# Optimization experiments

Hardware: AMD Instinct MI355X
Metric: run time of the kernel (lower is better)

## Reference

```python
import jax, jax.numpy as jnp
import numpy as np

EPS = 1e-8


def setup_inputs() -> dict:
    key = jax.random.key(0)
    k1, k2, k3 = jax.random.split(key, 3)
    N, M, D = 200000, 64, 128
    X = jax.random.normal(k1, (N, D), dtype=jnp.float32)
    r = jax.random.uniform(k2, (N, M), dtype=jnp.float32)
    mus = jax.random.normal(k3, (M, D), dtype=jnp.float32)
    return {"X": X, "r": r, "mus": mus}


def _pairwise_l2_sim(X, mus):
    # sim = -||x - mu||_2, computed via the Gram trick to avoid an [N,M,D] intermediate
    x2 = jnp.sum(X * X, axis=-1, keepdims=True)          # [N,1]
    m2 = jnp.sum(mus * mus, axis=-1)[None, :]            # [1,M]
    sq = x2 + m2 - 2.0 * (X @ mus.T)                     # [N,M]
    return -jnp.sqrt(jnp.maximum(sq, 0.0))


def reference(X, r, mus):
    N = X.shape[0]
    sim = _pairwise_l2_sim(X, mus)                       # [N,M]
    sim_z = -jnp.log(jax.nn.sigmoid(sim) + EPS)          # [N,M]
    loss = jnp.sum(r * sim_z) / N
    return loss
```

## Files before the change

kernel.cpp:

```cpp
#include <hip/hip_runtime.h>
#include <math.h>

#define D_DIM 128
#define M_CLUSTERS 64
#define BLOCK 256
#define GRIDB 1024
#define W_TOTAL 4096
#define RBLOCK 1024

typedef __bf16 bf16x8 __attribute__((ext_vector_type(8)));
typedef float f32x4 __attribute__((ext_vector_type(4)));

union B8 { int4 i; bf16x8 b; };
union F4 { float4 v; float f[4]; };

__device__ __forceinline__ float zval(float sq) {
    float dd = sqrtf(fmaxf(sq, 0.0f));
    float sg = __fdividef(1.0f, 1.0f + __expf(dd));
    return -__logf(sg + 1e-8f);
}

__device__ __forceinline__ void gload16(const void* g, void* l) {
    __builtin_amdgcn_global_load_lds(
        (const __attribute__((address_space(1))) unsigned int*)g,
        (__attribute__((address_space(3))) unsigned int*)l, 16, 0, 0);
}

__global__ void iso_prep(const float4* __restrict__ mus4, int4* __restrict__ muB4,
                         float* __restrict__ m2) {
    const int f = blockIdx.x * 256 + threadIdx.x;
    float4 v0 = mus4[f * 2 + 0];
    float4 v1 = mus4[f * 2 + 1];
    B8 p;
    p.b[0] = (__bf16)v0.x; p.b[1] = (__bf16)v0.y;
    p.b[2] = (__bf16)v0.z; p.b[3] = (__bf16)v0.w;
    p.b[4] = (__bf16)v1.x; p.b[5] = (__bf16)v1.y;
    p.b[6] = (__bf16)v1.z; p.b[7] = (__bf16)v1.w;
    muB4[f] = p.i;
    if (blockIdx.x == 0 && threadIdx.x < M_CLUSTERS) {
        const float4* mv = mus4 + threadIdx.x * (D_DIM / 4);
        float s = 0.f;
#pragma unroll
        for (int d = 0; d < D_DIM / 4; ++d) {
            float4 v = mv[d];
            s = fmaf(v.x, v.x, s);
            s = fmaf(v.y, v.y, s);
            s = fmaf(v.z, v.z, s);
            s = fmaf(v.w, v.w, s);
        }
        m2[threadIdx.x] = s;
    }
}

__global__ __launch_bounds__(BLOCK, 4) void iso_main(
        const float* __restrict__ X, const float* __restrict__ r,
        const int4* __restrict__ muB4, const float* __restrict__ m2g,
        float* __restrict__ partials, int N) {
    __shared__ __align__(16) char bs[16384];

    const int tid = threadIdx.x;
    const int lane = tid & 63;
    const int la = lane & 15;
    const int lg = lane >> 4;
    const int w = tid >> 6;
    const int gid = blockIdx.x * 4 + w;
    const int ntiles = N >> 4;

#pragma unroll
    for (int i = 0; i < 4; ++i) {
        int kchunk = w * 4 + i;
        int c = kchunk * 4 + (lane >> 4);
        int slot = (lane & 15) ^ (c & 7);
        gload16(muB4 + c * 16 + slot, bs + kchunk * 1024);
    }
    F4 m2r[4];
    {
        const float4* mp = (const float4*)m2g + lg;
#pragma unroll
        for (int cb = 0; cb < 4; ++cb) m2r[cb].v = mp[cb * 4];
    }
    float4 xA[8], xB[8];
    {
        const char* xb = (const char*)X + (size_t)gid * 8192 +
                         (size_t)la * 512 + lg * 32;
        xA[0] = *(const float4*)(xb + 0);   xA[1] = *(const float4*)(xb + 16);
        xA[2] = *(const float4*)(xb + 128); xA[3] = *(const float4*)(xb + 144);
        xA[4] = *(const float4*)(xb + 256); xA[5] = *(const float4*)(xb + 272);
        xA[6] = *(const float4*)(xb + 384); xA[7] = *(const float4*)(xb + 400);
    }
    __syncthreads();

    float partial = 0.f;

    auto run_stage = [&](int k, const float4 (&cur)[8], float4 (&nxt)[8]) {
        const int tk = gid + k * W_TOTAL;
        const bool valid = tk < ntiles;
        const size_t ta = valid ? (size_t)tk : (size_t)gid;

        F4 rv[4];
        const char* rb = (const char*)r + ta * 4096 + (size_t)la * 256 + lg * 16;
        rv[0].v = *(const float4*)(rb + 0);
        rv[1].v = *(const float4*)(rb + 64);
        rv[2].v = *(const float4*)(rb + 128);
        rv[3].v = *(const float4*)(rb + 192);

        int tn = gid + (k + 1) * W_TOTAL;
        if (tn >= ntiles) tn = gid;
        const char* xb = (const char*)X + (size_t)tn * 8192 +
                         (size_t)la * 512 + lg * 32;
        nxt[0] = *(const float4*)(xb + 0);   nxt[1] = *(const float4*)(xb + 16);
        nxt[2] = *(const float4*)(xb + 128); nxt[3] = *(const float4*)(xb + 144);
        nxt[4] = *(const float4*)(xb + 256); nxt[5] = *(const float4*)(xb + 272);
        nxt[6] = *(const float4*)(xb + 384); nxt[7] = *(const float4*)(xb + 400);

        __builtin_amdgcn_sched_barrier(0);

        B8 xf[4];
        float x2 = 0.f;
#pragma unroll
        for (int kk = 0; kk < 4; ++kk) {
            float4 a = cur[2 * kk], b = cur[2 * kk + 1];
            xf[kk].b[0] = (__bf16)a.x; xf[kk].b[1] = (__bf16)a.y;
            xf[kk].b[2] = (__bf16)a.z; xf[kk].b[3] = (__bf16)a.w;
            xf[kk].b[4] = (__bf16)b.x; xf[kk].b[5] = (__bf16)b.y;
            xf[kk].b[6] = (__bf16)b.z; xf[kk].b[7] = (__bf16)b.w;
            x2 = fmaf(a.x, a.x, x2); x2 = fmaf(a.y, a.y, x2);
            x2 = fmaf(a.z, a.z, x2); x2 = fmaf(a.w, a.w, x2);
            x2 = fmaf(b.x, b.x, x2); x2 = fmaf(b.y, b.y, x2);
            x2 = fmaf(b.z, b.z, x2); x2 = fmaf(b.w, b.w, x2);
        }

        f32x4 acc[4];
#pragma unroll
        for (int cb = 0; cb < 4; ++cb)
#pragma unroll
            for (int q = 0; q < 4; ++q) acc[cb][q] = 0.f;
#pragma unroll
        for (int kk = 0; kk < 4; ++kk)
#pragma unroll
            for (int cb = 0; cb < 4; ++cb) {
                int c = cb * 16 + la;
                B8 bfr;
                bfr.i = *(const int4*)(bs + c * 256 +
                                       (((kk * 4 + lg) ^ (c & 7)) * 16));
                acc[cb] = __builtin_amdgcn_mfma_f32_16x16x32_bf16(
                    bfr.b, xf[kk].b, acc[cb], 0, 0, 0);
            }

        x2 += __shfl_xor(x2, 16, 64);
        x2 += __shfl_xor(x2, 32, 64);

        float p = 0.f;
#pragma unroll
        for (int cb = 0; cb < 4; ++cb)
#pragma unroll
            for (int q = 0; q < 4; ++q) {
                float sq = x2 + m2r[cb].f[q] - 2.0f * acc[cb][q];
                p = fmaf(rv[cb].f[q], zval(sq), p);
            }
        if (valid) partial += p;
    };

    run_stage(0, xA, xB);
    run_stage(1, xB, xA);
    run_stage(2, xA, xB);
    run_stage(3, xB, xA);

#pragma unroll
    for (int off = 32; off > 0; off >>= 1)
        partial += __shfl_down(partial, off, 64);
    if (lane == 0) partials[gid] = partial;
}

__global__ __launch_bounds__(RBLOCK) void iso_reduce(
        const float* __restrict__ partials, int n,
        float* __restrict__ out, float invN) {
    float s = 0.f;
    for (int i = threadIdx.x; i < n; i += RBLOCK) s += partials[i];
#pragma unroll
    for (int off = 32; off > 0; off >>= 1)
        s += __shfl_down(s, off, 64);
    __shared__ float wsum[RBLOCK / 64];
    const int lane = threadIdx.x & 63;
    const int wid = threadIdx.x >> 6;
    if (lane == 0) wsum[wid] = s;
    __syncthreads();
    if (threadIdx.x == 0) {
        float t = 0.f;
#pragma unroll
        for (int j = 0; j < RBLOCK / 64; ++j) t += wsum[j];
        out[0] = t * invN;
    }
}

extern "C" void kernel_launch(void* const* d_in, const int* in_sizes, int n_in,
                              void* d_out, int out_size, void* d_ws, size_t ws_size,
                              hipStream_t stream) {
    const float* X = (const float*)d_in[0];
    const float* r = (const float*)d_in[1];
    const float* mus = (const float*)d_in[2];
    const int N = in_sizes[0] / D_DIM;

    int4* muB4 = (int4*)d_ws;
    float* m2 = (float*)((char*)d_ws + 16384);
    float* partials = m2 + M_CLUSTERS;

    hipLaunchKernelGGL(iso_prep, dim3(4), dim3(256), 0, stream,
                       (const float4*)mus, muB4, m2);
    hipLaunchKernelGGL(iso_main, dim3(GRIDB), dim3(BLOCK), 0, stream,
                       X, r, muB4, m2, partials, N);
    hipLaunchKernelGGL(iso_reduce, dim3(1), dim3(RBLOCK), 0, stream,
                       partials, W_TOTAL, (float*)d_out, 1.0f / (float)N);
}
```

Before: 41.32 us.

## Fuse prep and reduce into main kernel with last-block atomic reduction

Each block now converts mus to bf16 into LDS and computes the squared norms itself, which removes the separate prep kernel. The final sum is done by the last block to finish, detected with an atomic counter, which removes the separate reduce kernel. The last stage also stops issuing the useless X prefetch. Every block repeats the 32KB mus conversion, and a memset launch is added to reset the counter.

```diff
diff --git a/kernel.cpp b/kernel.cpp
--- a/kernel.cpp
+++ b/kernel.cpp
@@ -6,7 +6,6 @@
 #define BLOCK 256
 #define GRIDB 1024
 #define W_TOTAL 4096
-#define RBLOCK 1024
 
 typedef __bf16 bf16x8 __attribute__((ext_vector_type(8)));
 typedef float f32x4 __attribute__((ext_vector_type(4)));
@@ -20,65 +19,22 @@
     return -__logf(sg + 1e-8f);
 }
 
-__device__ __forceinline__ void gload16(const void* g, void* l) {
-    __builtin_amdgcn_global_load_lds(
-        (const __attribute__((address_space(1))) unsigned int*)g,
-        (__attribute__((address_space(3))) unsigned int*)l, 16, 0, 0);
-}
-
-__global__ void iso_prep(const float4* __restrict__ mus4, int4* __restrict__ muB4,
-                         float* __restrict__ m2) {
-    const int f = blockIdx.x * 256 + threadIdx.x;
-    float4 v0 = mus4[f * 2 + 0];
-    float4 v1 = mus4[f * 2 + 1];
-    B8 p;
-    p.b[0] = (__bf16)v0.x; p.b[1] = (__bf16)v0.y;
-    p.b[2] = (__bf16)v0.z; p.b[3] = (__bf16)v0.w;
-    p.b[4] = (__bf16)v1.x; p.b[5] = (__bf16)v1.y;
-    p.b[6] = (__bf16)v1.z; p.b[7] = (__bf16)v1.w;
-    muB4[f] = p.i;
-    if (blockIdx.x == 0 && threadIdx.x < M_CLUSTERS) {
-        const float4* mv = mus4 + threadIdx.x * (D_DIM / 4);
-        float s = 0.f;
-#pragma unroll
-        for (int d = 0; d < D_DIM / 4; ++d) {
-            float4 v = mv[d];
-            s = fmaf(v.x, v.x, s);
-            s = fmaf(v.y, v.y, s);
-            s = fmaf(v.z, v.z, s);
-            s = fmaf(v.w, v.w, s);
-        }
-        m2[threadIdx.x] = s;
-    }
-}
-
 __global__ __launch_bounds__(BLOCK, 4) void iso_main(
         const float* __restrict__ X, const float* __restrict__ r,
-        const int4* __restrict__ muB4, const float* __restrict__ m2g,
-        float* __restrict__ partials, int N) {
-    __shared__ __align__(16) char bs[16384];
+        const float4* __restrict__ mus4, float* __restrict__ partials,
+        unsigned int* __restrict__ cnt, float* __restrict__ out,
+        int N, float invN) {
+    __shared__ __align__(16) char bs[16384 + 256];
+    __shared__ float wsum[4];
+    __shared__ unsigned int isLast;
 
     const int tid = threadIdx.x;
     const int lane = tid & 63;
     const int la = lane & 15;
     const int lg = lane >> 4;
-    const int w = tid >> 6;
-    const int gid = blockIdx.x * 4 + w;
+    const int gid = blockIdx.x * 4 + (tid >> 6);
     const int ntiles = N >> 4;
 
-#pragma unroll
-    for (int i = 0; i < 4; ++i) {
-        int kchunk = w * 4 + i;
-        int c = kchunk * 4 + (lane >> 4);
-        int slot = (lane & 15) ^ (c & 7);
-        gload16(muB4 + c * 16 + slot, bs + kchunk * 1024);
-    }
-    F4 m2r[4];
-    {
-        const float4* mp = (const float4*)m2g + lg;
-#pragma unroll
-        for (int cb = 0; cb < 4; ++cb) m2r[cb].v = mp[cb * 4];
-    }
     float4 xA[8], xB[8];
     {
         const char* xb = (const char*)X + (size_t)gid * 8192 +
@@ -88,11 +44,43 @@
         xA[4] = *(const float4*)(xb + 256); xA[5] = *(const float4*)(xb + 272);
         xA[6] = *(const float4*)(xb + 384); xA[7] = *(const float4*)(xb + 400);
     }
+
+    {
+        float msq = 0.f;
+#pragma unroll
+        for (int i = 0; i < 4; ++i) {
+            int f = tid * 4 + i;
+            int c = f >> 4, sl = f & 15;
+            float4 v0 = mus4[f * 2 + 0];
+            float4 v1 = mus4[f * 2 + 1];
+            B8 p;
+            p.b[0] = (__bf16)v0.x; p.b[1] = (__bf16)v0.y;
+            p.b[2] = (__bf16)v0.z; p.b[3] = (__bf16)v0.w;
+            p.b[4] = (__bf16)v1.x; p.b[5] = (__bf16)v1.y;
+            p.b[6] = (__bf16)v1.z; p.b[7] = (__bf16)v1.w;
+            *(int4*)(bs + c * 256 + ((sl ^ (c & 7)) * 16)) = p.i;
+            msq = fmaf(v0.x, v0.x, msq); msq = fmaf(v0.y, v0.y, msq);
+            msq = fmaf(v0.z, v0.z, msq); msq = fmaf(v0.w, v0.w, msq);
+            msq = fmaf(v1.x, v1.x, msq); msq = fmaf(v1.y, v1.y, msq);
+            msq = fmaf(v1.z, v1.z, msq); msq = fmaf(v1.w, v1.w, msq);
+        }
+        msq += __shfl_xor(msq, 1, 64);
+        msq += __shfl_xor(msq, 2, 64);
+        if ((tid & 3) == 0)
+            ((float*)(bs + 16384))[tid >> 2] = msq;
+    }
     __syncthreads();
 
+    F4 m2r[4];
+    {
+        const float4* m2p = (const float4*)(bs + 16384);
+#pragma unroll
+        for (int cb = 0; cb < 4; ++cb) m2r[cb].v = m2p[cb * 4 + lg];
+    }
+
     float partial = 0.f;
 
-    auto run_stage = [&](int k, const float4 (&cur)[8], float4 (&nxt)[8]) {
+    auto run_stage = [&](int k, bool pf, const float4 (&cur)[8], float4 (&nxt)[8]) {
         const int tk = gid + k * W_TOTAL;
         const bool valid = tk < ntiles;
         const size_t ta = valid ? (size_t)tk : (size_t)gid;
@@ -104,15 +92,21 @@
         rv[2].v = *(const float4*)(rb + 128);
         rv[3].v = *(const float4*)(rb + 192);
 
-        int tn = gid + (k + 1) * W_TOTAL;
-        if (tn >= ntiles) tn = gid;
-        const char* xb = (const char*)X + (size_t)tn * 8192 +
-                         (size_t)la * 512 + lg * 32;
-        nxt[0] = *(const float4*)(xb + 0);   nxt[1] = *(const float4*)(xb + 16);
-        nxt[2] = *(const float4*)(xb + 128); nxt[3] = *(const float4*)(xb + 144);
-        nxt[4] = *(const float4*)(xb + 256); nxt[5] = *(const float4*)(xb + 272);
-        nxt[6] = *(const float4*)(xb + 384); nxt[7] = *(const float4*)(xb + 400);
-
+        if (pf) {
+            int tn = gid + (k + 1) * W_TOTAL;
+            if (tn < ntiles) {
+                const char* xb = (const char*)X + (size_t)tn * 8192 +
+                                 (size_t)la * 512 + lg * 32;
+                nxt[0] = *(const float4*)(xb + 0);
+                nxt[1] = *(const float4*)(xb + 16);
+                nxt[2] = *(const float4*)(xb + 128);
+                nxt[3] = *(const float4*)(xb + 144);
+                nxt[4] = *(const float4*)(xb + 256);
+                nxt[5] = *(const float4*)(xb + 272);
+                nxt[6] = *(const float4*)(xb + 384);
+                nxt[7] = *(const float4*)(xb + 400);
+            }
+        }
         __builtin_amdgcn_sched_barrier(0);
 
         B8 xf[4];
@@ -161,35 +155,36 @@
         if (valid) partial += p;
     };
 
-    run_stage(0, xA, xB);
-    run_stage(1, xB, xA);
-    run_stage(2, xA, xB);
-    run_stage(3, xB, xA);
+    run_stage(0, true, xA, xB);
+    run_stage(1, true, xB, xA);
+    run_stage(2, true, xA, xB);
+    run_stage(3, false, xB, xA);
 
 #pragma unroll
     for (int off = 32; off > 0; off >>= 1)
         partial += __shfl_down(partial, off, 64);
     if (lane == 0) partials[gid] = partial;
-}
-
-__global__ __launch_bounds__(RBLOCK) void iso_reduce(
-        const float* __restrict__ partials, int n,
-        float* __restrict__ out, float invN) {
-    float s = 0.f;
-    for (int i = threadIdx.x; i < n; i += RBLOCK) s += partials[i];
-#pragma unroll
-    for (int off = 32; off > 0; off >>= 1)
-        s += __shfl_down(s, off, 64);
-    __shared__ float wsum[RBLOCK / 64];
-    const int lane = threadIdx.x & 63;
-    const int wid = threadIdx.x >> 6;
-    if (lane == 0) wsum[wid] = s;
+
+    __threadfence();
     __syncthreads();
-    if (threadIdx.x == 0) {
-        float t = 0.f;
-#pragma unroll
-        for (int j = 0; j < RBLOCK / 64; ++j) t += wsum[j];
-        out[0] = t * invN;
+    if (tid == 0) {
+        unsigned int old = atomicAdd(cnt, 1u);
+        isLast = (old == GRIDB - 1) ? 1u : 0u;
+    }
+    __syncthreads();
+    if (isLast) {
+        __threadfence();
+        float s = 0.f;
+        for (int i = tid; i < W_TOTAL; i += BLOCK) s += partials[i];
+#pragma unroll
+        for (int off = 32; off > 0; off >>= 1)
+            s += __shfl_down(s, off, 64);
+        if (lane == 0) wsum[tid >> 6] = s;
+        __syncthreads();
+        if (tid == 0) {
+            out[0] = (wsum[0] + wsum[1] + wsum[2] + wsum[3]) * invN;
+            *cnt = 0;
+        }
     }
 }
 
@@ -201,14 +196,11 @@
     const float* mus = (const float*)d_in[2];
     const int N = in_sizes[0] / D_DIM;
 
-    int4* muB4 = (int4*)d_ws;
-    float* m2 = (float*)((char*)d_ws + 16384);
-    float* partials = m2 + M_CLUSTERS;
-
-    hipLaunchKernelGGL(iso_prep, dim3(4), dim3(256), 0, stream,
-                       (const float4*)mus, muB4, m2);
+    float* partials = (float*)d_ws;
+    unsigned int* cnt = (unsigned int*)((char*)d_ws + W_TOTAL * sizeof(float));
+
+    hipMemsetAsync(cnt, 0, sizeof(unsigned int), stream);
     hipLaunchKernelGGL(iso_main, dim3(GRIDB), dim3(BLOCK), 0, stream,
-                       X, r, muB4, m2, partials, N);
-    hipLaunchKernelGGL(iso_reduce, dim3(1), dim3(RBLOCK), 0, stream,
-                       partials, W_TOTAL, (float*)d_out, 1.0f / (float)N);
+                       X, r, (const float4*)mus, partials, cnt, (float*)d_out,
+                       N, 1.0f / (float)N);
 }
```

Result: slower. 150.8 us, median of 6 (+264.9%).

## Double waves per block and drop register prefetch of next X tile

Applied to the files above, without the earlier changes.

Doubles the block to 8 waves and the total wave count to 8192, so each wave handles 2 tiles instead of 4. The explicit register double-buffering of the next X tile and the sched_barrier are removed, and tiles are loaded inside a simple loop with an early break. The m2 values are staged through shared memory instead of being held in registers across the kernel. The intent is to lower register pressure and raise occupancy so latency is hidden by more resident waves rather than by software prefetch, at the cost of less per-wave overlap of loads with compute.

```diff
diff --git a/kernel.cpp b/kernel.cpp
--- a/kernel.cpp
+++ b/kernel.cpp
@@ -3,9 +3,9 @@
 
 #define D_DIM 128
 #define M_CLUSTERS 64
-#define BLOCK 256
+#define BLOCK 512
 #define GRIDB 1024
-#define W_TOTAL 4096
+#define W_TOTAL 8192
 #define RBLOCK 1024
 
 typedef __bf16 bf16x8 __attribute__((ext_vector_type(8)));
@@ -52,74 +52,57 @@
     }
 }
 
-__global__ __launch_bounds__(BLOCK, 4) void iso_main(
+__global__ __launch_bounds__(BLOCK, 8) void iso_main(
         const float* __restrict__ X, const float* __restrict__ r,
         const int4* __restrict__ muB4, const float* __restrict__ m2g,
         float* __restrict__ partials, int N) {
-    __shared__ __align__(16) char bs[16384];
+    __shared__ __align__(16) char bs[16384 + 256];
 
     const int tid = threadIdx.x;
     const int lane = tid & 63;
     const int la = lane & 15;
     const int lg = lane >> 4;
     const int w = tid >> 6;
-    const int gid = blockIdx.x * 4 + w;
+    const int gid = blockIdx.x * 8 + w;
     const int ntiles = N >> 4;
 
 #pragma unroll
-    for (int i = 0; i < 4; ++i) {
-        int kchunk = w * 4 + i;
+    for (int i = 0; i < 2; ++i) {
+        int kchunk = w * 2 + i;
         int c = kchunk * 4 + (lane >> 4);
         int slot = (lane & 15) ^ (c & 7);
         gload16(muB4 + c * 16 + slot, bs + kchunk * 1024);
     }
-    F4 m2r[4];
-    {
-        const float4* mp = (const float4*)m2g + lg;
-#pragma unroll
-        for (int cb = 0; cb < 4; ++cb) m2r[cb].v = mp[cb * 4];
-    }
-    float4 xA[8], xB[8];
-    {
-        const char* xb = (const char*)X + (size_t)gid * 8192 +
-                         (size_t)la * 512 + lg * 32;
-        xA[0] = *(const float4*)(xb + 0);   xA[1] = *(const float4*)(xb + 16);
-        xA[2] = *(const float4*)(xb + 128); xA[3] = *(const float4*)(xb + 144);
-        xA[4] = *(const float4*)(xb + 256); xA[5] = *(const float4*)(xb + 272);
-        xA[6] = *(const float4*)(xb + 384); xA[7] = *(const float4*)(xb + 400);
-    }
+    if (tid < M_CLUSTERS) ((float*)(bs + 16384))[tid] = m2g[tid];
     __syncthreads();
 
     float partial = 0.f;
 
-    auto run_stage = [&](int k, const float4 (&cur)[8], float4 (&nxt)[8]) {
+    for (int k = 0; k < 2; ++k) {
         const int tk = gid + k * W_TOTAL;
-        const bool valid = tk < ntiles;
-        const size_t ta = valid ? (size_t)tk : (size_t)gid;
+        if (tk >= ntiles) break;
+
+        const char* xb = (const char*)X + (size_t)tk * 8192 +
+                         (size_t)la * 512 + lg * 32;
+        float4 xv[8];
+        xv[0] = *(const float4*)(xb + 0);   xv[1] = *(const float4*)(xb + 16);
+        xv[2] = *(const float4*)(xb + 128); xv[3] = *(const float4*)(xb + 144);
+        xv[4] = *(const float4*)(xb + 256); xv[5] = *(const float4*)(xb + 272);
+        xv[6] = *(const float4*)(xb + 384); xv[7] = *(const float4*)(xb + 400);
 
         F4 rv[4];
-        const char* rb = (const char*)r + ta * 4096 + (size_t)la * 256 + lg * 16;
+        const char* rb = (const char*)r + (size_t)tk * 4096 +
+                         (size_t)la * 256 + lg * 16;
         rv[0].v = *(const float4*)(rb + 0);
         rv[1].v = *(const float4*)(rb + 64);
         rv[2].v = *(const float4*)(rb + 128);
         rv[3].v = *(const float4*)(rb + 192);
 
-        int tn = gid + (k + 1) * W_TOTAL;
-        if (tn >= ntiles) tn = gid;
-        const char* xb = (const char*)X + (size_t)tn * 8192 +
-                         (size_t)la * 512 + lg * 32;
-        nxt[0] = *(const float4*)(xb + 0);   nxt[1] = *(const float4*)(xb + 16);
-        nxt[2] = *(const float4*)(xb + 128); nxt[3] = *(const float4*)(xb + 144);
-        nxt[4] = *(const float4*)(xb + 256); nxt[5] = *(const float4*)(xb + 272);
-        nxt[6] = *(const float4*)(xb + 384); nxt[7] = *(const float4*)(xb + 400);
-
-        __builtin_amdgcn_sched_barrier(0);
-
         B8 xf[4];
         float x2 = 0.f;
 #pragma unroll
         for (int kk = 0; kk < 4; ++kk) {
-            float4 a = cur[2 * kk], b = cur[2 * kk + 1];
+            float4 a = xv[2 * kk], b = xv[2 * kk + 1];
             xf[kk].b[0] = (__bf16)a.x; xf[kk].b[1] = (__bf16)a.y;
             xf[kk].b[2] = (__bf16)a.z; xf[kk].b[3] = (__bf16)a.w;
             xf[kk].b[4] = (__bf16)b.x; xf[kk].b[5] = (__bf16)b.y;
@@ -150,21 +133,19 @@
         x2 += __shfl_xor(x2, 16, 64);
         x2 += __shfl_xor(x2, 32, 64);
 
-        float p = 0.f;
+        F4 m2r[4];
+        const float4* m2p = (const float4*)(bs + 16384);
+#pragma unroll
+        for (int cb = 0; cb < 4; ++cb) m2r[cb].v = m2p[cb * 4 + lg];
+
 #pragma unroll
         for (int cb = 0; cb < 4; ++cb)
 #pragma unroll
             for (int q = 0; q < 4; ++q) {
                 float sq = x2 + m2r[cb].f[q] - 2.0f * acc[cb][q];
-                p = fmaf(rv[cb].f[q], zval(sq), p);
+                partial = fmaf(rv[cb].f[q], zval(sq), partial);
             }
-        if (valid) partial += p;
-    };
-
-    run_stage(0, xA, xB);
-    run_stage(1, xB, xA);
-    run_stage(2, xA, xB);
-    run_stage(3, xB, xA);
+    }
 
 #pragma unroll
     for (int off = 32; off > 0; off >>= 1)
```

Result: slower. 45.23 us (+9.5%).
